# Kernel optimization log

Measured on AMD Instinct MI355X. Metric: run time of the kernel, lower is better.

Reference implementation:

```python
import jax, jax.numpy as jnp
import numpy as np

N = 100000
IN_C, HID_C, OUT_C = 128, 128, 128
E = 3200000


def gcn_conv(x, src, dst, W, b, num_nodes):
    # Linear transform first (smaller feature dim already), then normalized scatter-add.
    h = x @ W  # [N, out]
    # symmetric normalization with self-loops already included in (src, dst)
    deg = jax.ops.segment_sum(jnp.ones_like(dst, dtype=h.dtype), dst, num_segments=num_nodes)
    dinv = jnp.where(deg > 0, jax.lax.rsqrt(deg), 0.0)  # deg^{-1/2}
    norm = dinv[src] * dinv[dst]  # [E_total]
    msgs = h[src] * norm[:, None]  # gather + scale, [E_total, out]
    out = jax.ops.segment_sum(msgs, dst, num_segments=num_nodes)  # scatter-add
    return out + b


def add_self_loops(edge_index, num_nodes):
    loop = jnp.arange(num_nodes, dtype=edge_index.dtype)
    src = jnp.concatenate([edge_index[0], loop])
    dst = jnp.concatenate([edge_index[1], loop])
    return src, dst


def setup_inputs() -> dict:
    key = jax.random.key(0)
    k1, k2, k3, k4, k5 = jax.random.split(key, 5)
    x = jax.random.normal(k1, (N, IN_C), dtype=jnp.float32)
    edge_index = jax.random.randint(k2, (2, E), 0, N, dtype=jnp.int64)
    # Glorot-ish init for GCN weights
    W1 = jax.random.normal(k3, (IN_C, HID_C), dtype=jnp.float32) * (1.0 / np.sqrt(IN_C))
    b1 = jnp.zeros((HID_C,), dtype=jnp.float32)
    W2 = jax.random.normal(k4, (HID_C, OUT_C), dtype=jnp.float32) * (1.0 / np.sqrt(HID_C))
    b2 = jnp.zeros((OUT_C,), dtype=jnp.float32)
    return {"x": x, "edge_index": edge_index, "W1": W1, "b1": b1, "W2": W2, "b2": b2}


def reference(x, edge_index, W1, b1, W2, b2):
    src, dst = add_self_loops(edge_index, N)
    h = gcn_conv(x, src, dst, W1, b1, N)
    h = jax.nn.relu(h)
    out = gcn_conv(h, src, dst, W2, b2, N)
    return out
```

## Files before the change

### kernel.cpp

```cpp
#include <hip/hip_runtime.h>


#define NPB 128
#define NBMAX 1024
#define EPT 64
#define PART_TILE (256 * EPT)

typedef unsigned short ushort_t;
typedef __attribute__((ext_vector_type(8))) short short8;
typedef __attribute__((ext_vector_type(4))) float f32x4;

__device__ __forceinline__ unsigned short f32_to_bf16_rne(float x) {
    unsigned int v = __float_as_uint(x);
    unsigned int r = v + 0x7fffu + ((v >> 16) & 1u);
    return (unsigned short)(r >> 16);
}

__global__ void k_zero(int* __restrict__ p, int n) {
    int i = blockIdx.x * blockDim.x + threadIdx.x;
    if (i < n) p[i] = 0;
}

__global__ __launch_bounds__(256) void k_wprep(
    const float* __restrict__ W1, const float* __restrict__ W2,
    ushort_t* __restrict__ Wp1, ushort_t* __restrict__ Wp2) {
    int idx = blockIdx.x * 256 + threadIdx.x;
    int which = idx >> 14;
    int e = idx & 16383;
    int n = e & 127, k = e >> 7;
    const float* W = which ? W2 : W1;
    ushort_t* Wp = which ? Wp2 : Wp1;
    Wp[n * 128 + k] = f32_to_bf16_rne(W[k * 128 + n]);
}

__global__ __launch_bounds__(256) void k_bucket_hist(
    const int* __restrict__ dst, int* __restrict__ bucket_count,
    int e, int n, int total) {
    __shared__ int hist[NBMAX];
    int nb = (n + NPB - 1) >> 7;
    int t = threadIdx.x;
    for (int k = t; k < nb; k += 256) hist[k] = 0;
    __syncthreads();
    int stride = gridDim.x * 256;
    for (int i = blockIdx.x * 256 + t; i < total; i += stride) {
        int d = (i < e) ? dst[i] : (i - e);
        atomicAdd(&hist[d >> 7], 1);
    }
    __syncthreads();
    for (int k = t; k < nb; k += 256) {
        int c = hist[k];
        if (c) atomicAdd(&bucket_count[k], c);
    }
}

__global__ __launch_bounds__(256) void k_bucket_scan(
    const int* __restrict__ bucket_count, int* __restrict__ bucket_ptr,
    int* __restrict__ bucket_cursor, int nb, int total) {
    __shared__ int sd[256];
    int t = threadIdx.x;
    int c[4];
#pragma unroll
    for (int j = 0; j < 4; j++) {
        int k = t * 4 + j;
        c[j] = (k < nb) ? bucket_count[k] : 0;
    }
    int s = c[0] + c[1] + c[2] + c[3];
    sd[t] = s;
    __syncthreads();
    for (int off = 1; off < 256; off <<= 1) {
        int v = (t >= off) ? sd[t - off] : 0;
        __syncthreads();
        sd[t] += v;
        __syncthreads();
    }
    int pre = sd[t] - s;
#pragma unroll
    for (int j = 0; j < 4; j++) {
        int k = t * 4 + j;
        if (k < nb) { bucket_ptr[k] = pre; bucket_cursor[k] = pre; }
        pre += c[j];
    }
    if (t == 255) bucket_ptr[nb] = total;
}

__global__ __launch_bounds__(256) void k_partition(
    const int* __restrict__ src, const int* __restrict__ dst,
    int* __restrict__ bucket_cursor, unsigned int* __restrict__ pairs,
    int e, int n, int total) {
    __shared__ int hist[NBMAX];
    __shared__ int base[NBMAX];
    int nb = (n + NPB - 1) >> 7;
    int t = threadIdx.x;
    int t0 = blockIdx.x * PART_TILE;
    for (int k = t; k < nb; k += 256) hist[k] = 0;
    __syncthreads();
#pragma unroll 4
    for (int j = 0; j < EPT; j++) {
        int i = t0 + j * 256 + t;
        if (i < total) {
            int d = (i < e) ? dst[i] : (i - e);
            atomicAdd(&hist[d >> 7], 1);
        }
    }
    __syncthreads();
    for (int k = t; k < nb; k += 256) {
        int c = hist[k];
        base[k] = c ? atomicAdd(&bucket_cursor[k], c) : 0;
        hist[k] = 0;
    }
    __syncthreads();
#pragma unroll 4
    for (int j = 0; j < EPT; j++) {
        int i = t0 + j * 256 + t;
        if (i < total) {
            int s, d;
            if (i < e) { s = src[i]; d = dst[i]; }
            else       { s = i - e;  d = s; }
            int b = d >> 7;
            int off = atomicAdd(&hist[b], 1);
            pairs[base[b] + off] = (unsigned int)s | ((unsigned int)(d & 127) << 17);
        }
    }
}

__global__ __launch_bounds__(256) void k_build(
    const unsigned int* __restrict__ pairs, const int* __restrict__ bucket_ptr,
    int* __restrict__ row_ptr, int* __restrict__ srcs,
    float* __restrict__ dinv, int n) {
    __shared__ int cnt[NPB];
    __shared__ int scn[NPB];
    __shared__ int cur[NPB];
    int b = blockIdx.x;
    int t = threadIdx.x;
    int node0 = b << 7;
    int p0 = bucket_ptr[b], p1 = bucket_ptr[b + 1];
    if (t < NPB) cnt[t] = 0;
    __syncthreads();
    for (int i = p0 + t; i < p1; i += 256) {
        int dlow = (int)(pairs[i] >> 17) & 127;
        atomicAdd(&cnt[dlow], 1);
    }
    __syncthreads();
    if (t < NPB) scn[t] = cnt[t];
    __syncthreads();
    for (int off = 1; off < NPB; off <<= 1) {
        int v = (t < NPB && t >= off) ? scn[t - off] : 0;
        __syncthreads();
        if (t < NPB) scn[t] += v;
        __syncthreads();
    }
    if (t < NPB) {
        int incl = scn[t];
        int excl = incl - cnt[t];
        int start = p0 + excl;
        cur[t] = start;
        int node = node0 + t;
        if (node < n) {
            row_ptr[node] = start;
            dinv[node] = rsqrtf((float)cnt[t]);
            if (node == n - 1) row_ptr[n] = p0 + incl;
        }
    }
    __syncthreads();
    for (int i = p0 + t; i < p1; i += 256) {
        unsigned int pr = pairs[i];
        int pos = atomicAdd(&cur[(pr >> 17) & 127], 1);
        srcs[pos] = (int)(pr & 0x1FFFFu);
    }
}

template <bool ABF16>
__global__ __launch_bounds__(256) void k_gemm_mfma(
    const void* __restrict__ Araw, const ushort_t* __restrict__ Wp,
    const float* __restrict__ dinv, ushort_t* __restrict__ G, int M) {
    __shared__ char smem[ABF16 ? (64 * 136 * 2) : (64 * 132 * 4)];
    float (*Af32)[132] = (float (*)[132])smem;
    ushort_t (*Au16)[136] = (ushort_t (*)[136])smem;

    int t = threadIdx.x;
    int row0 = blockIdx.x * 64;

    {
        int r = t >> 2;
        int seg = (t & 3) * 32;
        int gr = row0 + r; if (gr >= M) gr = M - 1;
        if constexpr (!ABF16) {
            const float* ap = (const float*)Araw + (size_t)gr * 128 + seg;
#pragma unroll
            for (int j = 0; j < 8; j++) {
                float4 v = ((const float4*)ap)[j];
                *(float4*)&Af32[r][seg + j * 4] = v;
            }
        } else {
            const ushort_t* ap = (const ushort_t*)Araw + (size_t)gr * 128 + seg;
#pragma unroll
            for (int j = 0; j < 4; j++) {
                uint4 v = ((const uint4*)ap)[j];
                *(uint4*)&Au16[r][seg + j * 8] = v;
            }
        }
    }
    __syncthreads();

    int wv = t >> 6;
    int lane = t & 63;
    int m = lane & 15;
    int quad = lane >> 4;
    int lrow = wv * 16 + m;

    f32x4 acc[8];
#pragma unroll
    for (int c = 0; c < 8; c++) acc[c] = (f32x4){0.f, 0.f, 0.f, 0.f};

#pragma unroll
    for (int ks = 0; ks < 4; ks++) {
        int kb = ks * 32 + quad * 8;
        short8 ahi, alo;
        if constexpr (!ABF16) {
            float xs[8];
#pragma unroll
            for (int j = 0; j < 8; j++) xs[j] = Af32[lrow][kb + j];
#pragma unroll
            for (int j = 0; j < 8; j++) {
                unsigned short h = f32_to_bf16_rne(xs[j]);
                ahi[j] = (short)h;
                float hf = __uint_as_float((unsigned int)h << 16);
                alo[j] = (short)f32_to_bf16_rne(xs[j] - hf);
            }
        } else {
            ahi = *(const short8*)&Au16[lrow][kb];
        }
#pragma unroll
        for (int c = 0; c < 8; c++) {
            short8 b8 = *(const short8*)(Wp + (size_t)(c * 16 + m) * 128 + kb);
            acc[c] = __builtin_amdgcn_mfma_f32_16x16x32_bf16(ahi, b8, acc[c], 0, 0, 0);
            if constexpr (!ABF16)
                acc[c] = __builtin_amdgcn_mfma_f32_16x16x32_bf16(alo, b8, acc[c], 0, 0, 0);
        }
    }

    int rbase = row0 + wv * 16 + quad * 4;
#pragma unroll
    for (int reg = 0; reg < 4; reg++) {
        int gr = rbase + reg;
        if (gr < M) {
            float dv = dinv[gr];
#pragma unroll
            for (int c = 0; c < 8; c++) {
                G[(size_t)gr * 128 + c * 16 + m] = f32_to_bf16_rne(acc[c][reg] * dv);
            }
        }
    }
}

template <int RELU, int OUTBF16>
__global__ __launch_bounds__(256) void k_aggregate(
    const int* __restrict__ row_ptr, const int* __restrict__ srcs,
    const ushort_t* __restrict__ G, const float* __restrict__ dinv,
    const float* __restrict__ bias, void* __restrict__ OutRaw, int n) {
    int wid = (blockIdx.x * 256 + threadIdx.x) >> 6;
    int lane = threadIdx.x & 63;
    if (wid >= n) return;
    int beg = row_ptr[wid], end = row_ptr[wid + 1];
    int c = lane * 2;
    float a0 = 0.f, a1 = 0.f;
    int p = beg;
    for (; p + 4 <= end; p += 4) {
        int s0 = srcs[p], s1 = srcs[p + 1], s2 = srcs[p + 2], s3 = srcs[p + 3];
        unsigned int u0 = *(const unsigned int*)(G + (size_t)s0 * 128 + c);
        unsigned int u1 = *(const unsigned int*)(G + (size_t)s1 * 128 + c);
        unsigned int u2 = *(const unsigned int*)(G + (size_t)s2 * 128 + c);
        unsigned int u3 = *(const unsigned int*)(G + (size_t)s3 * 128 + c);
        a0 += __uint_as_float(u0 << 16) + __uint_as_float(u1 << 16) +
              __uint_as_float(u2 << 16) + __uint_as_float(u3 << 16);
        a1 += __uint_as_float(u0 & 0xffff0000u) + __uint_as_float(u1 & 0xffff0000u) +
              __uint_as_float(u2 & 0xffff0000u) + __uint_as_float(u3 & 0xffff0000u);
    }
    for (; p < end; p++) {
        int s = srcs[p];
        unsigned int u = *(const unsigned int*)(G + (size_t)s * 128 + c);
        a0 += __uint_as_float(u << 16);
        a1 += __uint_as_float(u & 0xffff0000u);
    }
    float dv = dinv[wid];
    a0 = fmaf(a0, dv, bias[c]);
    a1 = fmaf(a1, dv, bias[c + 1]);
    if (RELU) { a0 = fmaxf(a0, 0.f); a1 = fmaxf(a1, 0.f); }
    if (OUTBF16) {
        unsigned int u = (unsigned int)f32_to_bf16_rne(a0) |
                         ((unsigned int)f32_to_bf16_rne(a1) << 16);
        ((unsigned int*)OutRaw)[(size_t)wid * 64 + lane] = u;
    } else {
        *(float2*)((float*)OutRaw + (size_t)wid * 128 + c) = make_float2(a0, a1);
    }
}

extern "C" void kernel_launch(void* const* d_in, const int* in_sizes, int n_in,
                              void* d_out, int out_size, void* d_ws, size_t ws_size,
                              hipStream_t stream) {
    const float* x  = (const float*)d_in[0];
    const int*   ei = (const int*)d_in[1];
    const float* W1 = (const float*)d_in[2];
    const float* b1 = (const float*)d_in[3];
    const float* W2 = (const float*)d_in[4];
    const float* b2 = (const float*)d_in[5];
    float* out = (float*)d_out;

    const int C = 128;
    const int N = in_sizes[0] / C;
    const int E = in_sizes[1] / 2;
    const int* src = ei;
    const int* dst = ei + E;
    const int total = E + N;
    const int nb = (N + NPB - 1) >> 7;

    char* ws = (char*)d_ws;
    size_t off = 0;
    auto alloc = [&](size_t bytes) -> void* {
        void* p = ws + off;
        off = (off + bytes + 511) & ~(size_t)511;
        return p;
    };
    int*   bucket_count  = (int*)alloc((size_t)(nb + 1) * 4);
    int*   bucket_ptr    = (int*)alloc((size_t)(nb + 1) * 4);
    int*   bucket_cursor = (int*)alloc((size_t)(nb + 1) * 4);
    int*   row_ptr       = (int*)alloc(((size_t)N + 1) * 4);
    float* dinv          = (float*)alloc((size_t)N * 4);
    int*   srcs          = (int*)alloc((size_t)total * 4);
    ushort_t* Wp1        = (ushort_t*)alloc(128 * 128 * 2);
    ushort_t* Wp2        = (ushort_t*)alloc(128 * 128 * 2);
    ushort_t* gbuf       = (ushort_t*)alloc((size_t)N * C * 2);
    size_t abytes = (size_t)N * C * 2;
    size_t pbytes = (size_t)total * 4;
    void*  shared = alloc(abytes > pbytes ? abytes : pbytes);
    ushort_t* act = (ushort_t*)shared;
    unsigned int* pairs = (unsigned int*)shared;

    k_wprep<<<128, 256, 0, stream>>>(W1, W2, Wp1, Wp2);
    k_zero<<<(nb + 255) / 256, 256, 0, stream>>>(bucket_count, nb);
    k_bucket_hist<<<256, 256, 0, stream>>>(dst, bucket_count, E, N, total);
    k_bucket_scan<<<1, 256, 0, stream>>>(bucket_count, bucket_ptr, bucket_cursor, nb, total);
    k_partition<<<(total + PART_TILE - 1) / PART_TILE, 256, 0, stream>>>(
        src, dst, bucket_cursor, pairs, E, N, total);
    k_build<<<nb, 256, 0, stream>>>(pairs, bucket_ptr, row_ptr, srcs, dinv, N);

    int gemm_blocks = (N + 63) / 64;
    k_gemm_mfma<false><<<gemm_blocks, 256, 0, stream>>>(x, Wp1, dinv, gbuf, N);
    k_aggregate<1, 1><<<(N + 3) / 4, 256, 0, stream>>>(row_ptr, srcs, gbuf, dinv, b1, act, N);

    k_gemm_mfma<true><<<gemm_blocks, 256, 0, stream>>>(act, Wp2, dinv, gbuf, N);
    k_aggregate<0, 0><<<(N + 3) / 4, 256, 0, stream>>>(row_ptr, srcs, gbuf, dinv, b2, out, N);
}
```

Before: 547.5 us.

## Fuse layer-1 aggregation with layer-2 GEMM and restructure edge partitioning

```diff
diff --git a/kernel.cpp b/kernel.cpp
--- a/kernel.cpp
+++ b/kernel.cpp
@@ -14,11 +14,6 @@
     unsigned int v = __float_as_uint(x);
     unsigned int r = v + 0x7fffu + ((v >> 16) & 1u);
     return (unsigned short)(r >> 16);
-}
-
-__global__ void k_zero(int* __restrict__ p, int n) {
-    int i = blockIdx.x * blockDim.x + threadIdx.x;
-    if (i < n) p[i] = 0;
 }
 
 __global__ __launch_bounds__(256) void k_wprep(
@@ -33,67 +28,15 @@
     Wp[n * 128 + k] = f32_to_bf16_rne(W[k * 128 + n]);
 }
 
-__global__ __launch_bounds__(256) void k_bucket_hist(
-    const int* __restrict__ dst, int* __restrict__ bucket_count,
-    int e, int n, int total) {
+__global__ __launch_bounds__(256) void k_hist_tiles(
+    const int* __restrict__ dst, int* __restrict__ C,
+    int e, int nbp, int total) {
     __shared__ int hist[NBMAX];
-    int nb = (n + NPB - 1) >> 7;
-    int t = threadIdx.x;
-    for (int k = t; k < nb; k += 256) hist[k] = 0;
-    __syncthreads();
-    int stride = gridDim.x * 256;
-    for (int i = blockIdx.x * 256 + t; i < total; i += stride) {
-        int d = (i < e) ? dst[i] : (i - e);
-        atomicAdd(&hist[d >> 7], 1);
-    }
-    __syncthreads();
-    for (int k = t; k < nb; k += 256) {
-        int c = hist[k];
-        if (c) atomicAdd(&bucket_count[k], c);
-    }
-}
-
-__global__ __launch_bounds__(256) void k_bucket_scan(
-    const int* __restrict__ bucket_count, int* __restrict__ bucket_ptr,
-    int* __restrict__ bucket_cursor, int nb, int total) {
-    __shared__ int sd[256];
-    int t = threadIdx.x;
-    int c[4];
-#pragma unroll
-    for (int j = 0; j < 4; j++) {
-        int k = t * 4 + j;
-        c[j] = (k < nb) ? bucket_count[k] : 0;
-    }
-    int s = c[0] + c[1] + c[2] + c[3];
-    sd[t] = s;
-    __syncthreads();
-    for (int off = 1; off < 256; off <<= 1) {
-        int v = (t >= off) ? sd[t - off] : 0;
-        __syncthreads();
-        sd[t] += v;
-        __syncthreads();
-    }
-    int pre = sd[t] - s;
-#pragma unroll
-    for (int j = 0; j < 4; j++) {
-        int k = t * 4 + j;
-        if (k < nb) { bucket_ptr[k] = pre; bucket_cursor[k] = pre; }
-        pre += c[j];
-    }
-    if (t == 255) bucket_ptr[nb] = total;
-}
-
-__global__ __launch_bounds__(256) void k_partition(
-    const int* __restrict__ src, const int* __restrict__ dst,
-    int* __restrict__ bucket_cursor, unsigned int* __restrict__ pairs,
-    int e, int n, int total) {
-    __shared__ int hist[NBMAX];
-    __shared__ int base[NBMAX];
-    int nb = (n + NPB - 1) >> 7;
-    int t = threadIdx.x;
-    int t0 = blockIdx.x * PART_TILE;
-    for (int k = t; k < nb; k += 256) hist[k] = 0;
-    __syncthreads();
+    int t = threadIdx.x;
+    int tile = blockIdx.x;
+    for (int k = t; k < nbp; k += 256) hist[k] = 0;
+    __syncthreads();
+    int t0 = tile * PART_TILE;
 #pragma unroll 4
     for (int j = 0; j < EPT; j++) {
         int i = t0 + j * 256 + t;
@@ -103,12 +46,75 @@
         }
     }
     __syncthreads();
-    for (int k = t; k < nb; k += 256) {
-        int c = hist[k];
-        base[k] = c ? atomicAdd(&bucket_cursor[k], c) : 0;
-        hist[k] = 0;
-    }
-    __syncthreads();
+    int* row = C + (size_t)tile * nbp;
+    for (int k = t; k < nbp; k += 256) row[k] = hist[k];
+}
+
+__global__ __launch_bounds__(256) void k_col_scan(
+    int* __restrict__ C, int* __restrict__ colsum, int T, int nbp) {
+    int b = blockIdx.x * 256 + threadIdx.x;
+    if (b >= nbp) return;
+    int running = 0;
+    int t = 0;
+    for (; t + 8 <= T; t += 8) {
+        int v[8];
+#pragma unroll
+        for (int j = 0; j < 8; j++) v[j] = C[(size_t)(t + j) * nbp + b];
+#pragma unroll
+        for (int j = 0; j < 8; j++) {
+            C[(size_t)(t + j) * nbp + b] = running;
+            running += v[j];
+        }
+    }
+    for (; t < T; t++) {
+        int v = C[(size_t)t * nbp + b];
+        C[(size_t)t * nbp + b] = running;
+        running += v;
+    }
+    colsum[b] = running;
+}
+
+__global__ __launch_bounds__(256) void k_bucket_scan(
+    const int* __restrict__ colsum, int* __restrict__ bucket_ptr,
+    int nbp, int total) {
+    __shared__ int sd[256];
+    int t = threadIdx.x;
+    int c[4];
+#pragma unroll
+    for (int j = 0; j < 4; j++) {
+        int k = t * 4 + j;
+        c[j] = (k < nbp) ? colsum[k] : 0;
+    }
+    int s = c[0] + c[1] + c[2] + c[3];
+    sd[t] = s;
+    __syncthreads();
+    for (int off = 1; off < 256; off <<= 1) {
+        int v = (t >= off) ? sd[t - off] : 0;
+        __syncthreads();
+        sd[t] += v;
+        __syncthreads();
+    }
+    int pre = sd[t] - s;
+#pragma unroll
+    for (int j = 0; j < 4; j++) {
+        int k = t * 4 + j;
+        if (k < nbp) bucket_ptr[k] = pre;
+        pre += c[j];
+    }
+    if (t == 255) bucket_ptr[nbp] = total;
+}
+
+__global__ __launch_bounds__(256) void k_partition(
+    const int* __restrict__ src, const int* __restrict__ dst,
+    const int* __restrict__ C, const int* __restrict__ bucket_ptr,
+    unsigned int* __restrict__ pairs, int e, int nbp, int total) {
+    __shared__ int lcur[NBMAX];
+    int t = threadIdx.x;
+    int tile = blockIdx.x;
+    const int* row = C + (size_t)tile * nbp;
+    for (int k = t; k < nbp; k += 256) lcur[k] = row[k] + bucket_ptr[k];
+    __syncthreads();
+    int t0 = tile * PART_TILE;
 #pragma unroll 4
     for (int j = 0; j < EPT; j++) {
         int i = t0 + j * 256 + t;
@@ -117,8 +123,8 @@
             if (i < e) { s = src[i]; d = dst[i]; }
             else       { s = i - e;  d = s; }
             int b = d >> 7;
-            int off = atomicAdd(&hist[b], 1);
-            pairs[base[b] + off] = (unsigned int)s | ((unsigned int)(d & 127) << 17);
+            int off = atomicAdd(&lcur[b], 1);
+            pairs[off] = (unsigned int)s | ((unsigned int)(d & 127) << 17);
         }
     }
 }
@@ -169,44 +175,19 @@
     }
 }
 
-template <bool ABF16>
-__global__ __launch_bounds__(256) void k_gemm_mfma(
-    const void* __restrict__ Araw, const ushort_t* __restrict__ Wp,
+__global__ __launch_bounds__(256) void k_gemm1(
+    const float* __restrict__ A, const ushort_t* __restrict__ Wp,
     const float* __restrict__ dinv, ushort_t* __restrict__ G, int M) {
-    __shared__ char smem[ABF16 ? (64 * 136 * 2) : (64 * 132 * 4)];
-    float (*Af32)[132] = (float (*)[132])smem;
-    ushort_t (*Au16)[136] = (ushort_t (*)[136])smem;
-
     int t = threadIdx.x;
     int row0 = blockIdx.x * 64;
-
-    {
-        int r = t >> 2;
-        int seg = (t & 3) * 32;
-        int gr = row0 + r; if (gr >= M) gr = M - 1;
-        if constexpr (!ABF16) {
-            const float* ap = (const float*)Araw + (size_t)gr * 128 + seg;
-#pragma unroll
-            for (int j = 0; j < 8; j++) {
-                float4 v = ((const float4*)ap)[j];
-                *(float4*)&Af32[r][seg + j * 4] = v;
-            }
-        } else {
-            const ushort_t* ap = (const ushort_t*)Araw + (size_t)gr * 128 + seg;
-#pragma unroll
-            for (int j = 0; j < 4; j++) {
-                uint4 v = ((const uint4*)ap)[j];
-                *(uint4*)&Au16[r][seg + j * 8] = v;
-            }
-        }
-    }
-    __syncthreads();
-
     int wv = t >> 6;
     int lane = t & 63;
     int m = lane & 15;
     int quad = lane >> 4;
-    int lrow = wv * 16 + m;
+
+    int gr_row = row0 + wv * 16 + m;
+    int gcl = gr_row < M ? gr_row : M - 1;
+    const float* ap = A + (size_t)gcl * 128 + quad * 8;
 
     f32x4 acc[8];
 #pragma unroll
@@ -215,27 +196,22 @@
 #pragma unroll
     for (int ks = 0; ks < 4; ks++) {
         int kb = ks * 32 + quad * 8;
+        float xs[8];
+        *(float4*)&xs[0] = *(const float4*)(ap + ks * 32);
+        *(float4*)&xs[4] = *(const float4*)(ap + ks * 32 + 4);
         short8 ahi, alo;
-        if constexpr (!ABF16) {
-            float xs[8];
-#pragma unroll
-            for (int j = 0; j < 8; j++) xs[j] = Af32[lrow][kb + j];
-#pragma unroll
-            for (int j = 0; j < 8; j++) {
-                unsigned short h = f32_to_bf16_rne(xs[j]);
-                ahi[j] = (short)h;
-                float hf = __uint_as_float((unsigned int)h << 16);
-                alo[j] = (short)f32_to_bf16_rne(xs[j] - hf);
-            }
-        } else {
-            ahi = *(const short8*)&Au16[lrow][kb];
+#pragma unroll
+        for (int j = 0; j < 8; j++) {
+            unsigned short h = f32_to_bf16_rne(xs[j]);
+            ahi[j] = (short)h;
+            float hf = __uint_as_float((unsigned int)h << 16);
+            alo[j] = (short)f32_to_bf16_rne(xs[j] - hf);
         }
 #pragma unroll
         for (int c = 0; c < 8; c++) {
             short8 b8 = *(const short8*)(Wp + (size_t)(c * 16 + m) * 128 + kb);
             acc[c] = __builtin_amdgcn_mfma_f32_16x16x32_bf16(ahi, b8, acc[c], 0, 0, 0);
-            if constexpr (!ABF16)
-                acc[c] = __builtin_amdgcn_mfma_f32_16x16x32_bf16(alo, b8, acc[c], 0, 0, 0);
+            acc[c] = __builtin_amdgcn_mfma_f32_16x16x32_bf16(alo, b8, acc[c], 0, 0, 0);
         }
     }
 
@@ -246,18 +222,96 @@
         if (gr < M) {
             float dv = dinv[gr];
 #pragma unroll
-            for (int c = 0; c < 8; c++) {
+            for (int c = 0; c < 8; c++)
                 G[(size_t)gr * 128 + c * 16 + m] = f32_to_bf16_rne(acc[c][reg] * dv);
+        }
+    }
+}
+
+__global__ __launch_bounds__(256) void k_agg1_gemm2(
+    const int* __restrict__ row_ptr, const int* __restrict__ srcs,
+    const ushort_t* __restrict__ G1, const float* __restrict__ dinv,
+    const float* __restrict__ b1, const ushort_t* __restrict__ Wp2,
+    ushort_t* __restrict__ G2, int n) {
+    __shared__ unsigned int ActU[16][68];
+
+    int t = threadIdx.x;
+    int wv = t >> 6;
+    int lane = t & 63;
+    int base = blockIdx.x * 16;
+    int c = lane * 2;
+
+#pragma unroll
+    for (int i = 0; i < 4; i++) {
+        int nl = wv * 4 + i;
+        int node = base + nl;
+        float a0 = 0.f, a1 = 0.f;
+        if (node < n) {
+            int beg = row_ptr[node], end = row_ptr[node + 1];
+            int p = beg;
+            for (; p + 4 <= end; p += 4) {
+                int s0 = __builtin_nontemporal_load(&srcs[p]);
+                int s1 = __builtin_nontemporal_load(&srcs[p + 1]);
+                int s2 = __builtin_nontemporal_load(&srcs[p + 2]);
+                int s3 = __builtin_nontemporal_load(&srcs[p + 3]);
+                unsigned int u0 = *(const unsigned int*)(G1 + (size_t)s0 * 128 + c);
+                unsigned int u1 = *(const unsigned int*)(G1 + (size_t)s1 * 128 + c);
+                unsigned int u2 = *(const unsigned int*)(G1 + (size_t)s2 * 128 + c);
+                unsigned int u3 = *(const unsigned int*)(G1 + (size_t)s3 * 128 + c);
+                a0 += __uint_as_float(u0 << 16) + __uint_as_float(u1 << 16) +
+                      __uint_as_float(u2 << 16) + __uint_as_float(u3 << 16);
+                a1 += __uint_as_float(u0 & 0xffff0000u) + __uint_as_float(u1 & 0xffff0000u) +
+                      __uint_as_float(u2 & 0xffff0000u) + __uint_as_float(u3 & 0xffff0000u);
             }
-        }
-    }
-}
-
-template <int RELU, int OUTBF16>
-__global__ __launch_bounds__(256) void k_aggregate(
+            for (; p < end; p++) {
+                int s = __builtin_nontemporal_load(&srcs[p]);
+                unsigned int u = *(const unsigned int*)(G1 + (size_t)s * 128 + c);
+                a0 += __uint_as_float(u << 16);
+                a1 += __uint_as_float(u & 0xffff0000u);
+            }
+            float dv = dinv[node];
+            a0 = fmaxf(fmaf(a0, dv, b1[c]), 0.f);
+            a1 = fmaxf(fmaf(a1, dv, b1[c + 1]), 0.f);
+        }
+        ActU[nl][lane] = (unsigned int)f32_to_bf16_rne(a0) |
+                         ((unsigned int)f32_to_bf16_rne(a1) << 16);
+    }
+    __syncthreads();
+
+    int m = lane & 15;
+    int quad = lane >> 4;
+    f32x4 acc[2];
+    acc[0] = (f32x4){0.f, 0.f, 0.f, 0.f};
+    acc[1] = (f32x4){0.f, 0.f, 0.f, 0.f};
+#pragma unroll
+    for (int ks = 0; ks < 4; ks++) {
+        int kb = ks * 32 + quad * 8;
+        short8 a8 = *(const short8*)&ActU[m][ks * 16 + quad * 4];
+#pragma unroll
+        for (int cl = 0; cl < 2; cl++) {
+            int ct = wv * 2 + cl;
+            short8 b8 = *(const short8*)(Wp2 + (size_t)(ct * 16 + m) * 128 + kb);
+            acc[cl] = __builtin_amdgcn_mfma_f32_16x16x32_bf16(a8, b8, acc[cl], 0, 0, 0);
+        }
+    }
+#pragma unroll
+    for (int reg = 0; reg < 4; reg++) {
+        int gnode = base + quad * 4 + reg;
+        if (gnode < n) {
+            float dv = dinv[gnode];
+#pragma unroll
+            for (int cl = 0; cl < 2; cl++) {
+                int ch = (wv * 2 + cl) * 16 + m;
+                G2[(size_t)gnode * 128 + ch] = f32_to_bf16_rne(acc[cl][reg] * dv);
+            }
+        }
+    }
+}
+
+__global__ __launch_bounds__(256) void k_agg2(
     const int* __restrict__ row_ptr, const int* __restrict__ srcs,
     const ushort_t* __restrict__ G, const float* __restrict__ dinv,
-    const float* __restrict__ bias, void* __restrict__ OutRaw, int n) {
+    const float* __restrict__ bias, float* __restrict__ Out, int n) {
     int wid = (blockIdx.x * 256 + threadIdx.x) >> 6;
     int lane = threadIdx.x & 63;
     if (wid >= n) return;
@@ -266,7 +320,10 @@
     float a0 = 0.f, a1 = 0.f;
     int p = beg;
     for (; p + 4 <= end; p += 4) {
-        int s0 = srcs[p], s1 = srcs[p + 1], s2 = srcs[p + 2], s3 = srcs[p + 3];
+        int s0 = __builtin_nontemporal_load(&srcs[p]);
+        int s1 = __builtin_nontemporal_load(&srcs[p + 1]);
+        int s2 = __builtin_nontemporal_load(&srcs[p + 2]);
+        int s3 = __builtin_nontemporal_load(&srcs[p + 3]);
         unsigned int u0 = *(const unsigned int*)(G + (size_t)s0 * 128 + c);
         unsigned int u1 = *(const unsigned int*)(G + (size_t)s1 * 128 + c);
         unsigned int u2 = *(const unsigned int*)(G + (size_t)s2 * 128 + c);
@@ -277,7 +334,7 @@
               __uint_as_float(u2 & 0xffff0000u) + __uint_as_float(u3 & 0xffff0000u);
     }
     for (; p < end; p++) {
-        int s = srcs[p];
+        int s = __builtin_nontemporal_load(&srcs[p]);
         unsigned int u = *(const unsigned int*)(G + (size_t)s * 128 + c);
         a0 += __uint_as_float(u << 16);
         a1 += __uint_as_float(u & 0xffff0000u);
@@ -285,14 +342,9 @@
     float dv = dinv[wid];
     a0 = fmaf(a0, dv, bias[c]);
     a1 = fmaf(a1, dv, bias[c + 1]);
-    if (RELU) { a0 = fmaxf(a0, 0.f); a1 = fmaxf(a1, 0.f); }
-    if (OUTBF16) {
-        unsigned int u = (unsigned int)f32_to_bf16_rne(a0) |
-                         ((unsigned int)f32_to_bf16_rne(a1) << 16);
-        ((unsigned int*)OutRaw)[(size_t)wid * 64 + lane] = u;
-    } else {
-        *(float2*)((float*)OutRaw + (size_t)wid * 128 + c) = make_float2(a0, a1);
-    }
+    unsigned long long uv = ((unsigned long long)__float_as_uint(a1) << 32) |
+                            (unsigned long long)__float_as_uint(a0);
+    __builtin_nontemporal_store(uv, (unsigned long long*)(Out + (size_t)wid * 128 + c));
 }
 
 extern "C" void kernel_launch(void* const* d_in, const int* in_sizes, int n_in,
@@ -312,7 +364,8 @@
     const int* src = ei;
     const int* dst = ei + E;
     const int total = E + N;
-    const int nb = (N + NPB - 1) >> 7;
+    const int nbp = (N + NPB - 1) >> 7;
+    const int T = (total + PART_TILE - 1) / PART_TILE;
 
     char* ws = (char*)d_ws;
     size_t off = 0;
@@ -321,33 +374,31 @@
         off = (off + bytes + 511) & ~(size_t)511;
         return p;
     };
-    int*   bucket_count  = (int*)alloc((size_t)(nb + 1) * 4);
-    int*   bucket_ptr    = (int*)alloc((size_t)(nb + 1) * 4);
-    int*   bucket_cursor = (int*)alloc((size_t)(nb + 1) * 4);
-    int*   row_ptr       = (int*)alloc(((size_t)N + 1) * 4);
-    float* dinv          = (float*)alloc((size_t)N * 4);
-    int*   srcs          = (int*)alloc((size_t)total * 4);
-    ushort_t* Wp1        = (ushort_t*)alloc(128 * 128 * 2);
-    ushort_t* Wp2        = (ushort_t*)alloc(128 * 128 * 2);
-    ushort_t* gbuf       = (ushort_t*)alloc((size_t)N * C * 2);
-    size_t abytes = (size_t)N * C * 2;
-    size_t pbytes = (size_t)total * 4;
-    void*  shared = alloc(abytes > pbytes ? abytes : pbytes);
-    ushort_t* act = (ushort_t*)shared;
+    int*   Cmat       = (int*)alloc((size_t)T * nbp * 4);
+    int*   colsum     = (int*)alloc((size_t)nbp * 4);
+    int*   bucket_ptr = (int*)alloc((size_t)(nbp + 1) * 4);
+    int*   row_ptr    = (int*)alloc(((size_t)N + 1) * 4);
+    float* dinv       = (float*)alloc((size_t)N * 4);
+    int*   srcs       = (int*)alloc((size_t)total * 4);
+    ushort_t* Wp1     = (ushort_t*)alloc(128 * 128 * 2);
+    ushort_t* Wp2     = (ushort_t*)alloc(128 * 128 * 2);
+    ushort_t* G1      = (ushort_t*)alloc((size_t)N * C * 2);
+    size_t g2b = (size_t)N * C * 2, pb = (size_t)total * 4;
+    void* shared = alloc(g2b > pb ? g2b : pb);
+    ushort_t* G2 = (ushort_t*)shared;
     unsigned int* pairs = (unsigned int*)shared;
 
     k_wprep<<<128, 256, 0, stream>>>(W1, W2, Wp1, Wp2);
-    k_zero<<<(nb + 255) / 256, 256, 0, stream>>>(bucket_count, nb);
-    k_bucket_hist<<<256, 256, 0, stream>>>(dst, bucket_count, E, N, total);
-    k_bucket_scan<<<1, 256, 0, stream>>>(bucket_count, bucket_ptr, bucket_cursor, nb, total);
-    k_partition<<<(total + PART_TILE - 1) / PART_TILE, 256, 0, stream>>>(
-        src, dst, bucket_cursor, pairs, E, N, total);
-    k_build<<<nb, 256, 0, stream>>>(pairs, bucket_ptr, row_ptr, srcs, dinv, N);
-
-    int gemm_blocks = (N + 63) / 64;
-    k_gemm_mfma<false><<<gemm_blocks, 256, 0, stream>>>(x, Wp1, dinv, gbuf, N);
-    k_aggregate<1, 1><<<(N + 3) / 4, 256, 0, stream>>>(row_ptr, srcs, gbuf, dinv, b1, act, N);
-
-    k_gemm_mfma<true><<<gemm_blocks, 256, 0, stream>>>(act, Wp2, dinv, gbuf, N);
-    k_aggregate<0, 0><<<(N + 3) / 4, 256, 0, stream>>>(row_ptr, srcs, gbuf, dinv, b2, out, N);
-}
+    k_hist_tiles<<<T, 256, 0, stream>>>(dst, Cmat, E, nbp, total);
+    k_col_scan<<<(nbp + 255) / 256, 256, 0, stream>>>(Cmat, colsum, T, nbp);
+    k_bucket_scan<<<1, 256, 0, stream>>>(colsum, bucket_ptr, nbp, total);
+    k_partition<<<T, 256, 0, stream>>>(src, dst, Cmat, bucket_ptr, pairs, E, nbp, total);
+    k_build<<<nbp, 256, 0, stream>>>(pairs, bucket_ptr, row_ptr, srcs, dinv, N);
+
+    k_gemm1<<<(N + 63) / 64, 256, 0, stream>>>(x, Wp1, dinv, G1, N);
+
+    k_agg1_gemm2<<<(N + 15) / 16, 256, 0, stream>>>(
+        row_ptr, srcs, G1, dinv, b1, Wp2, G2, N);
+
+    k_agg2<<<(N + 3) / 4, 256, 0, stream>>>(row_ptr, srcs, G2, dinv, b2, out, N);
+}
```

Measured after the change: 594.1 us. +8.5%, slower.
